# Kernel optimization log

Hardware: AMD Instinct MI355X
Metric: run time of the kernel (lower is better)

Reference implementation:

```python
import jax, jax.numpy as jnp
import numpy as np

EPS = 1e-5


def layer_norm(x, g, b):
    mu = jnp.mean(x, axis=-1, keepdims=True)
    var = jnp.var(x, axis=-1, keepdims=True)
    return (x - mu) * jax.lax.rsqrt(var + EPS) * g + b


def setup_inputs() -> dict:
    key = jax.random.key(0)
    ks = jax.random.split(key, 10)
    B, N, D, H, DFF = 4, 2048, 384, 6, 2048
    s = lambda fan: 1.0 / np.sqrt(fan)
    return {
        "x": jax.random.normal(ks[0], (B, N, D), dtype=jnp.float32),
        "norm_g": jnp.ones((D,), jnp.float32),
        "norm_b": jnp.zeros((D,), jnp.float32),
        "w_qkv": jax.random.uniform(ks[1], (D, 3 * D), jnp.float32, -s(D), s(D)),
        "b_qkv": jax.random.uniform(ks[2], (3 * D,), jnp.float32, -s(D), s(D)),
        "w1": jax.random.uniform(ks[3], (D, DFF), jnp.float32, -s(D), s(D)),
        "b1": jax.random.uniform(ks[4], (DFF,), jnp.float32, -s(D), s(D)),
        "w2": jax.random.uniform(ks[5], (DFF, D), jnp.float32, -s(DFF), s(DFF)),
        "b2": jax.random.uniform(ks[6], (D,), jnp.float32, -s(DFF), s(DFF)),
    }


def reference(x, norm_g, norm_b, w_qkv, b_qkv, w1, b1, w2, b2):
    H = 6
    B, N, D = x.shape
    hd = D // H
    scale = hd ** -0.5

    # --- attention (pre-norm, shared LayerNorm params) ---
    out = layer_norm(x, norm_g, norm_b)
    qkv = out @ w_qkv + b_qkv                     # [B, N, 3D]
    q, k, v = jnp.split(qkv, 3, axis=-1)
    to_heads = lambda t: t.reshape(B, N, H, hd).transpose(0, 2, 1, 3)  # b h n d
    q, k, v = to_heads(q), to_heads(k), to_heads(v)
    scores = jnp.einsum('bhid,bhjd->bhij', q, k) * scale
    attn = jax.nn.softmax(scores, axis=-1)        # dropout is identity in eval
    att = jnp.einsum('bhij,bhjd->bhid', attn, v)  # [B, H, N, hd]
    att = att.transpose(0, 2, 1, 3).reshape(B, N, D)
    x2 = x + att

    # --- MLP (same shared LayerNorm) ---
    y = layer_norm(x2, norm_g, norm_b)
    h = jax.nn.gelu(y @ w1 + b1, approximate=False)  # torch F.gelu exact
    mlp = h @ w2 + b2
    return x2 + mlp
```

## Files before the change

kernel.cpp:

```cpp
#include <hip/hip_runtime.h>
#include <cstdint>
#include <cstddef>

#define DEV static __device__ __forceinline__

typedef __attribute__((ext_vector_type(8))) short short8;
typedef __attribute__((ext_vector_type(16))) float f32x16;
typedef __attribute__((ext_vector_type(4))) unsigned short u16x4;
typedef __attribute__((ext_vector_type(2))) unsigned short u16x2;

constexpr int kB = 4, kN = 2048, kD = 384, kH = 6, kDFF = 2048;
constexpr int kM = kB * kN;
constexpr int kBH = kB * kH;
constexpr float kQPre = 0.18033688011112042f;

DEV float exp2fast(float f) { return __builtin_amdgcn_exp2f(f); }

DEV unsigned short f2b(float f) {
  union { float fp; uint32_t u; } v; v.fp = f;
  return (unsigned short)((v.u + 0x7fffu + ((v.u >> 16) & 1u)) >> 16);
}

DEV void gload16(const unsigned short* g, unsigned short* l) {
  __builtin_amdgcn_global_load_lds(
      (const __attribute__((address_space(1))) unsigned int*)g,
      (__attribute__((address_space(3))) unsigned int*)l, 16, 0, 0);
}

DEV float gelu_fast(float x) {
  float t = exp2fast(x * (2.3022081f + 0.1029432f * x * x));
  return x - x * __builtin_amdgcn_rcpf(t + 1.0f);
}

__global__ __launch_bounds__(256) void k_pre(
    const float* __restrict__ wqkv, unsigned short* __restrict__ wqkvT,
    const float* __restrict__ w1,   unsigned short* __restrict__ w1T,
    const float* __restrict__ w2,   unsigned short* __restrict__ w2T,
    const float* __restrict__ x, const float* __restrict__ g,
    const float* __restrict__ bta, unsigned short* __restrict__ y) {
  const int tid = threadIdx.x;
  if (blockIdx.x >= 492) {
    int row  = (blockIdx.x - 492) * 4 + (tid >> 6);
    int lane = tid & 63;
    const float* xr = x + (size_t)row * kD;
    float4 a = *(const float4*)(xr + lane * 4);
    float2 c = *(const float2*)(xr + 256 + lane * 2);
    float s  = a.x + a.y + a.z + a.w + c.x + c.y;
    float ss = a.x*a.x + a.y*a.y + a.z*a.z + a.w*a.w + c.x*c.x + c.y*c.y;
#pragma unroll
    for (int m = 1; m < 64; m <<= 1) {
      s  += __shfl_xor(s,  m, 64);
      ss += __shfl_xor(ss, m, 64);
    }
    float mean = s * (1.0f / kD);
    float var  = ss * (1.0f / kD) - mean * mean;
    float r = rsqrtf(var + 1e-5f);
    float4 g4 = *(const float4*)(g + lane * 4);
    float2 g2 = *(const float2*)(g + 256 + lane * 2);
    float4 b4 = *(const float4*)(bta + lane * 4);
    float2 b2 = *(const float2*)(bta + 256 + lane * 2);
    unsigned short* yr = y + (size_t)row * kD;
    u16x4 o4;
    o4[0] = f2b((a.x - mean) * r * g4.x + b4.x);
    o4[1] = f2b((a.y - mean) * r * g4.y + b4.y);
    o4[2] = f2b((a.z - mean) * r * g4.z + b4.z);
    o4[3] = f2b((a.w - mean) * r * g4.w + b4.w);
    *(u16x4*)(yr + lane * 4) = o4;
    u16x2 o2;
    o2[0] = f2b((c.x - mean) * r * g2.x + b2.x);
    o2[1] = f2b((c.y - mean) * r * g2.y + b2.y);
    *(u16x2*)(yr + 256 + lane * 2) = o2;
    return;
  }
  __shared__ unsigned short t[64][66];
  int idx = blockIdx.x;
  const float* w; unsigned short* wT; int K, Nn, nbk;
  if (idx < 108)      { w = wqkv; wT = wqkvT; K = 384;  Nn = 1152; nbk = 6; }
  else if (idx < 300) { w = w1;   wT = w1T;   K = 384;  Nn = 2048; nbk = 6;  idx -= 108; }
  else                { w = w2;   wT = w2T;   K = 2048; Nn = 384;  nbk = 32; idx -= 300; }
  const int bk = idx % nbk, bn = idx / nbk;
  const int k0 = bk << 6, n0 = bn << 6;
  const int cl = tid & 63, rw = tid >> 6;
#pragma unroll
  for (int it = 0; it < 16; ++it) {
    int kk = it * 4 + rw;
    t[cl][kk] = f2b(w[(size_t)(k0 + kk) * Nn + n0 + cl]);
  }
  __syncthreads();
  const int kq = (tid & 15) << 2;
  const int nr = tid >> 4;
#pragma unroll
  for (int it = 0; it < 4; ++it) {
    int nn = it * 16 + nr;
    u16x4 v;
    v[0] = t[nn][kq]; v[1] = t[nn][kq + 1]; v[2] = t[nn][kq + 2]; v[3] = t[nn][kq + 3];
    *(u16x4*)&wT[(size_t)(n0 + nn) * K + k0 + kq] = v;
  }
}

__global__ __launch_bounds__(256) void k_layernorm(
    const float* __restrict__ x, const float* __restrict__ g,
    const float* __restrict__ bta, unsigned short* __restrict__ y) {
  int row  = blockIdx.x * 4 + (threadIdx.x >> 6);
  int lane = threadIdx.x & 63;
  const float* xr = x + (size_t)row * kD;
  float4 a = *(const float4*)(xr + lane * 4);
  float2 c = *(const float2*)(xr + 256 + lane * 2);
  float s  = a.x + a.y + a.z + a.w + c.x + c.y;
  float ss = a.x*a.x + a.y*a.y + a.z*a.z + a.w*a.w + c.x*c.x + c.y*c.y;
#pragma unroll
  for (int m = 1; m < 64; m <<= 1) {
    s  += __shfl_xor(s,  m, 64);
    ss += __shfl_xor(ss, m, 64);
  }
  float mean = s * (1.0f / kD);
  float var  = ss * (1.0f / kD) - mean * mean;
  float r = rsqrtf(var + 1e-5f);
  float4 g4 = *(const float4*)(g + lane * 4);
  float2 g2 = *(const float2*)(g + 256 + lane * 2);
  float4 b4 = *(const float4*)(bta + lane * 4);
  float2 b2 = *(const float2*)(bta + 256 + lane * 2);
  unsigned short* yr = y + (size_t)row * kD;
  u16x4 o4;
  o4[0] = f2b((a.x - mean) * r * g4.x + b4.x);
  o4[1] = f2b((a.y - mean) * r * g4.y + b4.y);
  o4[2] = f2b((a.z - mean) * r * g4.z + b4.z);
  o4[3] = f2b((a.w - mean) * r * g4.w + b4.w);
  *(u16x4*)(yr + lane * 4) = o4;
  u16x2 o2;
  o2[0] = f2b((c.x - mean) * r * g2.x + b2.x);
  o2[1] = f2b((c.y - mean) * r * g2.y + b2.y);
  *(u16x2*)(yr + 256 + lane * 2) = o2;
}

template <int MODE, int TM>
__global__ __launch_bounds__(256) void k_gemm(
    const unsigned short* __restrict__ A, const unsigned short* __restrict__ Bt,
    const float* __restrict__ bias, int K, int Nn, int nbm,
    unsigned short* __restrict__ oq, unsigned short* __restrict__ okk,
    unsigned short* __restrict__ ov, unsigned short* __restrict__ oh,
    const float* __restrict__ res, float* __restrict__ out) {
  constexpr int FI = 1;
  constexpr int FJ = (TM >= 64) ? 2 : 1;
  __shared__ unsigned short lA[2][TM * 64];
  __shared__ unsigned short lB[2][128 * 64];
  const int tid = threadIdx.x, wid = tid >> 6, lane = tid & 63;
  const int bm = blockIdx.x % nbm, bn = blockIdx.x / nbm;
  const int m0 = bm * TM, n0 = bn * 128;
  const int wr = (TM >= 64) ? (wid >> 1) : 0;
  const int wc = (TM >= 64) ? (wid & 1) : wid;
  const int wmo = wr * 32;
  const int wno = wc * (FJ * 32);
  const int l31 = lane & 31, lh = lane >> 5;
  const int rsw = l31 & 7;

  f32x16 acc[FI][FJ];
#pragma unroll
  for (int i = 0; i < FI; i++)
#pragma unroll
    for (int j = 0; j < FJ; j++)
#pragma unroll
      for (int r = 0; r < 16; r++) acc[i][j][r] = 0.f;

  const int srow = tid >> 3;
  const int sslot = tid & 7;

  auto stage = [&](int buf, int k0) {
#pragma unroll
    for (int p = 0; p < 4; p++) {
      int row = (p << 5) + srow;
      int sl  = (sslot ^ (row & 7)) << 3;
      gload16(Bt + (size_t)(n0 + row) * K + k0 + sl,
              &lB[buf][(row << 6) + (sslot << 3)]);
    }
#pragma unroll
    for (int p = 0; p < TM / 32; p++) {
      int row = (p << 5) + srow;
      int sl  = (sslot ^ (row & 7)) << 3;
      gload16(A + (size_t)(m0 + row) * K + k0 + sl,
              &lA[buf][(row << 6) + (sslot << 3)]);
    }
  };

  stage(0, 0);

  const int nkt = K >> 6;
  for (int kt = 0; kt < nkt; ++kt) {
    const int cur = kt & 1;
    __syncthreads();
    if (kt + 1 < nkt) stage(cur ^ 1, (kt + 1) << 6);
    short8 af[FI][4], bf[FJ][4];
#pragma unroll
    for (int i = 0; i < FI; i++)
#pragma unroll
      for (int ks = 0; ks < 4; ks++)
        af[i][ks] = *(const short8*)&lA[cur][((wmo + (i << 5) + l31) << 6) +
                                            ((((ks << 1) + lh) ^ rsw) << 3)];
#pragma unroll
    for (int j = 0; j < FJ; j++)
#pragma unroll
      for (int ks = 0; ks < 4; ks++)
        bf[j][ks] = *(const short8*)&lB[cur][((wno + (j << 5) + l31) << 6) +
                                            ((((ks << 1) + lh) ^ rsw) << 3)];
#pragma unroll
    for (int i = 0; i < FI; i++)
#pragma unroll
      for (int j = 0; j < FJ; j++)
#pragma unroll
        for (int ks = 0; ks < 4; ks++)
          acc[i][j] = __builtin_amdgcn_mfma_f32_32x32x16_bf16(af[i][ks], bf[j][ks],
                                                              acc[i][j], 0, 0, 0);
  }

#pragma unroll
  for (int i = 0; i < FI; i++) {
#pragma unroll
    for (int j = 0; j < FJ; j++) {
      int col = n0 + wno + (j << 5) + l31;
      float bv = bias[col];
#pragma unroll
      for (int reg = 0; reg < 16; ++reg) {
        int m = m0 + wmo + (i << 5) + (reg & 3) + ((reg >> 2) << 3) + (lh << 2);
        float cvl = acc[i][j][reg] + bv;
        if (MODE == 0) {
          int bI = m >> 11, nI = m & 2047;
          if (col < 384) {
            int hh = col >> 6, dd = col & 63;
            oq[(((size_t)bI * kH + hh) * kN + nI) * 64 + dd] = f2b(cvl * kQPre);
          } else if (col < 768) {
            int c2 = col - 384; int hh = c2 >> 6, dd = c2 & 63;
            okk[(((size_t)bI * kH + hh) * kN + nI) * 64 + dd] = f2b(cvl);
          } else {
            int c2 = col - 768; int hh = c2 >> 6, dd = c2 & 63;
            ov[(((size_t)bI * kH + hh) * 64 + dd) * kN + nI] = f2b(cvl);
          }
        } else if (MODE == 1) {
          oh[(size_t)m * kDFF + col] = f2b(gelu_fast(cvl));
        } else {
          size_t idx = (size_t)m * kD + col;
          out[idx] = res[idx] + cvl;
        }
      }
    }
  }
}

__global__ __launch_bounds__(256) void k_attn(
    const unsigned short* __restrict__ Q, const unsigned short* __restrict__ Kg,
    const unsigned short* __restrict__ Vt, const float* __restrict__ x,
    float* __restrict__ x2) {
  __shared__ unsigned short sh[4 * 4096];
  unsigned short* lK = sh;
  unsigned short* lV = sh + 8192;
  const int tid = threadIdx.x, wid = tid >> 6, lane = tid & 63;
  const int swz = (blockIdx.x & 7) * (gridDim.x >> 3) + (blockIdx.x >> 3);
  const int bh = swz >> 5, qt = swz & 31;
  const int b = bh / kH, h = bh - b * kH;
  const unsigned short* Qp = Q  + (size_t)bh * kN * 64;
  const unsigned short* Kp = Kg + (size_t)bh * kN * 64;
  const unsigned short* Vp = Vt + (size_t)bh * 64 * kN;
  const int l31 = lane & 31, lh = lane >> 5;
  const int qh = wid & 1, kvh = wid >> 1;
  const int q0 = qt * 64;
  const int rsw7 = l31 & 7;

  const int sr  = ((wid << 3) + (lane >> 3));
  const int scc = (lane & 7) << 3;

  short8 qb[4];
#pragma unroll
  for (int ks = 0; ks < 4; ++ks)
    qb[ks] = *(const short8*)(Qp + (size_t)(q0 + qh * 32 + l31) * 64 + ks * 16 + lh * 8);

  f32x16 o[2];
#pragma unroll
  for (int dt = 0; dt < 2; ++dt)
#pragma unroll
    for (int r = 0; r < 16; r++) o[dt][r] = 0.f;
  float l_r = 0.f;

  auto stage = [&](int buf, int t) {
#pragma unroll
    for (int p = 0; p < 2; p++) {
      int r = sr + (p << 5);
      int sl = ((lane & 7) ^ (r & 7)) << 3;
      gload16(Kp + (size_t)(t * 64 + r) * 64 + sl, &lK[buf * 4096 + (r << 6) + scc]);
      gload16(Vp + (size_t)r * kN + t * 64 + sl,   &lV[buf * 4096 + (r << 6) + scc]);
    }
  };

  stage(0, 0);

  constexpr int kNT = kN / 64;
  for (int t = 0; t < kNT; ++t) {
    const int cur = t & 1;
    __syncthreads();
    if (t + 1 < kNT) stage(cur ^ 1, t + 1);

    f32x16 s;
#pragma unroll
    for (int r = 0; r < 16; r++) s[r] = 0.f;
#pragma unroll
    for (int ks = 0; ks < 4; ++ks) {
      short8 kf = *(const short8*)&lK[cur * 4096 + ((kvh * 32 + l31) << 6) +
                                      ((((ks << 1) + lh) ^ rsw7) << 3)];
      s = __builtin_amdgcn_mfma_f32_32x32x16_bf16(kf, qb[ks], s, 0, 0, 0);
    }

    uint32_t Aw[4], Bw[4];
    float lsum = 0.f;
#pragma unroll
    for (int g = 0; g < 4; ++g) {
      float p0 = exp2fast(s[4 * g + 0]);
      float p1 = exp2fast(s[4 * g + 1]);
      float p2 = exp2fast(s[4 * g + 2]);
      float p3 = exp2fast(s[4 * g + 3]);
      lsum += (p0 + p1) + (p2 + p3);
      asm("v_cvt_pk_bf16_f32 %0, %1, %2" : "=v"(Aw[g]) : "v"(p0), "v"(p1));
      asm("v_cvt_pk_bf16_f32 %0, %1, %2" : "=v"(Bw[g]) : "v"(p2), "v"(p3));
    }
    l_r += lsum + __shfl_xor(lsum, 32, 64);

    short8 pb[2];
#pragma unroll
    for (int ks = 0; ks < 2; ++ks) {
      uint32_t cA = lh ? Aw[2 * ks + 1] : Aw[2 * ks];
      uint32_t cB = lh ? Bw[2 * ks + 1] : Bw[2 * ks];
      uint32_t dA = lh ? Aw[2 * ks] : Aw[2 * ks + 1];
      uint32_t dB = lh ? Bw[2 * ks] : Bw[2 * ks + 1];
      uint32_t sA = __shfl_xor(dA, 32, 64);
      uint32_t sB = __shfl_xor(dB, 32, 64);
      union { uint32_t u[4]; short8 s8; } bld;
      bld.u[0] = lh ? sA : cA;
      bld.u[1] = lh ? sB : cB;
      bld.u[2] = lh ? cA : sA;
      bld.u[3] = lh ? cB : sB;
      pb[ks] = bld.s8;
    }

#pragma unroll
    for (int dt = 0; dt < 2; ++dt) {
#pragma unroll
      for (int ks = 0; ks < 2; ++ks) {
        short8 va = *(const short8*)&lV[cur * 4096 + (((dt << 5) + l31) << 6) +
                        ((((kvh << 2) + (ks << 1) + lh) ^ rsw7) << 3)];
        o[dt] = __builtin_amdgcn_mfma_f32_32x32x16_bf16(va, pb[ks], o[dt], 0, 0, 0);
      }
    }
  }

  __syncthreads();
  float* fb = (float*)sh;
  float* lb = (float*)sh + 64 * 65;
  const int q = qh * 32 + l31;
  if (kvh == 1) {
#pragma unroll
    for (int dt = 0; dt < 2; ++dt)
#pragma unroll
      for (int reg = 0; reg < 16; ++reg) {
        int d = (dt << 5) + (reg & 3) + ((reg >> 2) << 3) + (lh << 2);
        fb[q * 65 + d] = o[dt][reg];
      }
    if (lh == 0) lb[q] = l_r;
  }
  __syncthreads();
  if (kvh == 0) {
#pragma unroll
    for (int dt = 0; dt < 2; ++dt)
#pragma unroll
      for (int reg = 0; reg < 16; ++reg) {
        int d = (dt << 5) + (reg & 3) + ((reg >> 2) << 3) + (lh << 2);
        fb[q * 65 + d] += o[dt][reg];
      }
    if (lh == 0) lb[q] += l_r;
  }
  __syncthreads();
  {
    int row = tid >> 2, dc = (tid & 3) << 4;
    float inv = __builtin_amdgcn_rcpf(lb[row]);
    size_t base = ((size_t)(b * kN + q0 + row)) * kD + h * 64 + dc;
#pragma unroll
    for (int i = 0; i < 16; i += 4) {
      float4 xv = *(const float4*)(x + base + i);
      float4 ov;
      ov.x = xv.x + fb[row * 65 + dc + i + 0] * inv;
      ov.y = xv.y + fb[row * 65 + dc + i + 1] * inv;
      ov.z = xv.z + fb[row * 65 + dc + i + 2] * inv;
      ov.w = xv.w + fb[row * 65 + dc + i + 3] * inv;
      *(float4*)(x2 + base + i) = ov;
    }
  }
}

extern "C" void kernel_launch(void* const* d_in, const int* in_sizes, int n_in,
                              void* d_out, int out_size, void* d_ws, size_t ws_size,
                              hipStream_t stream) {
  const float* x    = (const float*)d_in[0];
  const float* ng   = (const float*)d_in[1];
  const float* nb   = (const float*)d_in[2];
  const float* wqkv = (const float*)d_in[3];
  const float* bqkv = (const float*)d_in[4];
  const float* w1   = (const float*)d_in[5];
  const float* b1   = (const float*)d_in[6];
  const float* w2   = (const float*)d_in[7];
  const float* b2   = (const float*)d_in[8];
  float* out = (float*)d_out;

  char* p = (char*)d_ws;
  auto take = [&](size_t bytes) -> char* {
    char* r = p; p += (bytes + 255) & ~(size_t)255; return r;
  };
  unsigned short* y     = (unsigned short*)take((size_t)kM * kD * 2);
  unsigned short* wqkvT = (unsigned short*)take((size_t)3 * kD * kD * 2);
  unsigned short* w1T   = (unsigned short*)take((size_t)kDFF * kD * 2);
  unsigned short* w2T   = (unsigned short*)take((size_t)kD * kDFF * 2);
  unsigned short* Qw    = (unsigned short*)take((size_t)kM * kD * 2);
  unsigned short* Kw    = (unsigned short*)take((size_t)kM * kD * 2);
  unsigned short* Vtw   = (unsigned short*)take((size_t)kM * kD * 2);
  float*          x2    = (float*)take((size_t)kM * kD * 4);
  unsigned short* hbuf  = (unsigned short*)take((size_t)kM * kDFF * 2);

  k_pre<<<492 + kM / 4, 256, 0, stream>>>(wqkv, wqkvT, w1, w1T, w2, w2T,
                                          x, ng, nb, y);
  k_gemm<0, 64><<<128 * 9, 256, 0, stream>>>(y, wqkvT, bqkv, kD, 3 * kD, 128,
                                             Qw, Kw, Vtw, nullptr, nullptr, nullptr);
  k_attn<<<kBH * 32, 256, 0, stream>>>(Qw, Kw, Vtw, x, x2);
  k_layernorm<<<kM / 4, 256, 0, stream>>>(x2, ng, nb, y);
  k_gemm<1, 64><<<128 * 16, 256, 0, stream>>>(y, w1T, b1, kD, kDFF, 128,
                                              nullptr, nullptr, nullptr, hbuf, nullptr, nullptr);
  k_gemm<2, 32><<<256 * 3, 256, 0, stream>>>(hbuf, w2T, b2, kDFF, kD, 256,
                                             nullptr, nullptr, nullptr, nullptr, x2, out);
}
```

Before: 135.2 us.

## Load K/V fragments directly from global memory in attention, dropping LDS staging

The attention kernel no longer stages K and V tiles into double-buffered shared memory with async global-to-LDS loads and per-tile barriers. Each wave now reads its MFMA operand fragments for K and V straight from global memory, and shared memory is used only for the final cross-wave reduction. This removes the per-iteration __syncthreads and LDS traffic, and the smaller LDS footprint may raise occupancy. In exchange, tiles that were shared across waves are now fetched redundantly from global memory or cache. Load latency is also no longer hidden by explicit prefetch.

```diff
diff --git a/kernel.cpp b/kernel.cpp
--- a/kernel.cpp
+++ b/kernel.cpp
@@ -249,9 +249,7 @@
     const unsigned short* __restrict__ Q, const unsigned short* __restrict__ Kg,
     const unsigned short* __restrict__ Vt, const float* __restrict__ x,
     float* __restrict__ x2) {
-  __shared__ unsigned short sh[4 * 4096];
-  unsigned short* lK = sh;
-  unsigned short* lV = sh + 8192;
+  __shared__ float fb[64 * 65 + 64];
   const int tid = threadIdx.x, wid = tid >> 6, lane = tid & 63;
   const int swz = (blockIdx.x & 7) * (gridDim.x >> 3) + (blockIdx.x >> 3);
   const int bh = swz >> 5, qt = swz & 31;
@@ -262,10 +260,6 @@
   const int l31 = lane & 31, lh = lane >> 5;
   const int qh = wid & 1, kvh = wid >> 1;
   const int q0 = qt * 64;
-  const int rsw7 = l31 & 7;
-
-  const int sr  = ((wid << 3) + (lane >> 3));
-  const int scc = (lane & 7) << 3;
 
   short8 qb[4];
 #pragma unroll
@@ -279,31 +273,19 @@
     for (int r = 0; r < 16; r++) o[dt][r] = 0.f;
   float l_r = 0.f;
 
-  auto stage = [&](int buf, int t) {
-#pragma unroll
-    for (int p = 0; p < 2; p++) {
-      int r = sr + (p << 5);
-      int sl = ((lane & 7) ^ (r & 7)) << 3;
-      gload16(Kp + (size_t)(t * 64 + r) * 64 + sl, &lK[buf * 4096 + (r << 6) + scc]);
-      gload16(Vp + (size_t)r * kN + t * 64 + sl,   &lV[buf * 4096 + (r << 6) + scc]);
-    }
-  };
-
-  stage(0, 0);
+  const unsigned short* Kr = Kp + (size_t)(kvh * 32 + l31) * 64;
+  const unsigned short* Vr0 = Vp + (size_t)l31 * kN + kvh * 32;
+  const unsigned short* Vr1 = Vp + (size_t)(32 + l31) * kN + kvh * 32;
 
   constexpr int kNT = kN / 64;
   for (int t = 0; t < kNT; ++t) {
-    const int cur = t & 1;
-    __syncthreads();
-    if (t + 1 < kNT) stage(cur ^ 1, t + 1);
-
+    const unsigned short* kt = Kr + (size_t)t * 64 * 64;
     f32x16 s;
 #pragma unroll
     for (int r = 0; r < 16; r++) s[r] = 0.f;
 #pragma unroll
     for (int ks = 0; ks < 4; ++ks) {
-      short8 kf = *(const short8*)&lK[cur * 4096 + ((kvh * 32 + l31) << 6) +
-                                      ((((ks << 1) + lh) ^ rsw7) << 3)];
+      short8 kf = *(const short8*)(kt + ks * 16 + lh * 8);
       s = __builtin_amdgcn_mfma_f32_32x32x16_bf16(kf, qb[ks], s, 0, 0, 0);
     }
 
@@ -339,19 +321,15 @@
     }
 
 #pragma unroll
-    for (int dt = 0; dt < 2; ++dt) {
-#pragma unroll
-      for (int ks = 0; ks < 2; ++ks) {
-        short8 va = *(const short8*)&lV[cur * 4096 + (((dt << 5) + l31) << 6) +
-                        ((((kvh << 2) + (ks << 1) + lh) ^ rsw7) << 3)];
-        o[dt] = __builtin_amdgcn_mfma_f32_32x32x16_bf16(va, pb[ks], o[dt], 0, 0, 0);
-      }
-    }
-  }
-
-  __syncthreads();
-  float* fb = (float*)sh;
-  float* lb = (float*)sh + 64 * 65;
+    for (int ks = 0; ks < 2; ++ks) {
+      short8 va0 = *(const short8*)(Vr0 + t * 64 + ks * 16 + lh * 8);
+      short8 va1 = *(const short8*)(Vr1 + t * 64 + ks * 16 + lh * 8);
+      o[0] = __builtin_amdgcn_mfma_f32_32x32x16_bf16(va0, pb[ks], o[0], 0, 0, 0);
+      o[1] = __builtin_amdgcn_mfma_f32_32x32x16_bf16(va1, pb[ks], o[1], 0, 0, 0);
+    }
+  }
+
+  float* lb = fb + 64 * 65;
   const int q = qh * 32 + l31;
   if (kvh == 1) {
 #pragma unroll
```

After: 182.3 us. 1.35x slower.
